# Performance work log

Measured on AMD Instinct MI355X. Metric: run time of the kernel, lower is better.

The kernel has to match this reference:

```python
import jax, jax.numpy as jnp
import numpy as np

B, H, W = 4, 1024, 1024
V, F, T = 98304, 196608, 131072
EPS = 1e-8


def setup_inputs() -> dict:
    key = jax.random.key(0)
    k = jax.random.split(key, 6)
    # screen-space vertices: xy in pixel coords, z (depth) in [0.5, 5.5)
    xy = jax.random.uniform(k[0], (B, V, 2), dtype=jnp.float32) * jnp.array([W, H], jnp.float32)
    z = jax.random.uniform(k[1], (B, V, 1), dtype=jnp.float32) * 5.0 + 0.5
    v2d = jnp.concatenate([xy, z], axis=-1)
    vt = jax.random.uniform(k[2], (T, 2), dtype=jnp.float32)
    vi = jax.random.randint(k[3], (F, 3), 0, V, dtype=jnp.int32)
    vti = jax.random.randint(k[4], (F, 3), 0, T, dtype=jnp.int32)
    # -1 marks background pixels (mask), as in the original renderer
    index_img = jax.random.randint(k[5], (B, H, W), -1, F, dtype=jnp.int32)
    vn = jax.random.normal(jax.random.fold_in(key, 7), (B, V, 3), dtype=jnp.float32)
    return {"v2d": v2d, "vt": vt, "vi": vi, "vti": vti, "index_img": index_img, "vn": vn}


def _epsclamp(x):
    return jnp.where(x < 0, jnp.minimum(x, -EPS), jnp.maximum(x, EPS))


def _gather_b(table, idx):
    # table [B,N,C], idx [B,H,W] -> [B,H,W,C]
    return jax.vmap(lambda t, i: t[i])(table, idx)


def reference(v2d, vt, vi, vti, index_img, vn):
    h, w = index_img.shape[1], index_img.shape[2]
    pcy, pcx = jnp.meshgrid(jnp.arange(h, dtype=v2d.dtype), jnp.arange(w, dtype=v2d.dtype), indexing="ij")
    mask = index_img != -1                       # [B,H,W]
    fm = mask.astype(v2d.dtype)                  # [B,H,W]
    ii = jnp.maximum(index_img, 0)               # [B,H,W]

    vi_img = vi[ii]                              # [B,H,W,3] vertex ids per pixel
    p0 = _gather_b(v2d, vi_img[..., 0])          # [B,H,W,3]
    p1 = _gather_b(v2d, vi_img[..., 1])
    p2 = _gather_b(v2d, vi_img[..., 2])

    vec01 = p1 - p0
    vec02 = p2 - p0
    det = vec01[..., 0] * vec02[..., 1] - vec01[..., 1] * vec02[..., 0]
    denom = _epsclamp(det)
    px = pcx[None] - p0[..., 0]
    py = pcy[None] - p0[..., 1]
    l1 = (px * vec02[..., 1] - py * vec02[..., 0]) / denom
    l2 = (py * vec01[..., 0] - px * vec01[..., 1]) / denom
    l0 = 1.0 - l1 - l2

    w0 = 1.0 / _epsclamp(p0[..., 2])
    w1 = 1.0 / _epsclamp(p1[..., 2])
    w2 = 1.0 / _epsclamp(p2[..., 2])
    zi = 1.0 / _epsclamp(w0 * l0 + w1 * l1 + w2 * l2)
    b0 = w0 * l0 * zi
    b1 = w1 * l1 * zi
    b2 = w2 * l2 * zi
    bary_img = jnp.stack([b0, b1, b2], axis=-1) * fm[..., None]   # [B,H,W,3]

    vti_img = vti[ii]                            # [B,H,W,3]
    t0 = vt[vti_img[..., 0]]                     # [B,H,W,2] (shared uv table)
    t1 = vt[vti_img[..., 1]]
    t2 = vt[vti_img[..., 2]]
    vt_img = t0 * b0[..., None] + t1 * b1[..., None] + t2 * b2[..., None]

    depth_img = zi * fm

    base = jnp.stack([(pcx * 2 + 1) / w, (pcy * 2 + 1) / h], axis=-1) - 1.0  # [H,W,2]
    vt_img = base[None] + fm[..., None] * ((vt_img * 2 - 1) - base[None])    # lerp

    n0 = _gather_b(vn, vi_img[..., 0])
    n1 = _gather_b(vn, vi_img[..., 1])
    n2 = _gather_b(vn, vi_img[..., 2])
    vn_img = (n0 * bary_img[..., 0:1] + n1 * bary_img[..., 1:2] + n2 * bary_img[..., 2:3]) * fm[..., None]

    return depth_img, bary_img, vt_img, vn_img
```

## Files before the change

### kernel.cpp

```cpp
#include <hip/hip_runtime.h>


#define EPSV 1e-8f

__device__ __forceinline__ float epsclamp(float x) {
    return x < 0.0f ? fminf(x, -EPSV) : fmaxf(x, EPSV);
}

constexpr int Wd = 1024, Hd = 1024, Vd = 98304;
constexpr int NPIX = 1 << 22;
constexpr int PPB  = 1 << 20;

struct I3 { int a, b, c; };
struct F3 { float x, y, z; };

__device__ __forceinline__ int base_pixel_swz(int j, int tid) {
    const int xcd = j & 7;
    const int b = xcd >> 1;
    const int sub = ((j >> 3) << 1) + (j & 1);
    return b * PPB + sub * 1024 + tid * 4;
}

__global__ __launch_bounds__(256) void pass1(
    const float* __restrict__ v2d,
    const int*   __restrict__ vi,
    const int*   __restrict__ index_img,
    float* __restrict__ out)
{
#pragma clang fp contract(off)
    const int pb = base_pixel_swz(blockIdx.x, threadIdx.x);
    const int b = pb >> 20;

    const int4 iv = *reinterpret_cast<const int4*>(index_img + pb);
    const int idx[4] = { iv.x, iv.y, iv.z, iv.w };

    I3 ii[4];
#pragma unroll
    for (int k = 0; k < 4; ++k) {
        const int f = idx[k] < 0 ? 0 : idx[k];
        ii[k] = *reinterpret_cast<const I3*>(vi + 3 * (size_t)f);
    }

    const float* __restrict__ vb = v2d + (size_t)b * Vd * 3;
    F3 P0[4], P1[4], P2[4];
#pragma unroll
    for (int k = 0; k < 4; ++k) {
        P0[k] = *reinterpret_cast<const F3*>(vb + 3 * (size_t)ii[k].a);
        P1[k] = *reinterpret_cast<const F3*>(vb + 3 * (size_t)ii[k].b);
        P2[k] = *reinterpret_cast<const F3*>(vb + 3 * (size_t)ii[k].c);
    }

    float dep[4], b0m[4], b1m[4], b2m[4];
#pragma unroll
    for (int k = 0; k < 4; ++k) {
        const int p = pb + k;
        const int x = p & (Wd - 1);
        const int y = (p >> 10) & (Hd - 1);
        const float fm = (idx[k] != -1) ? 1.0f : 0.0f;

        const float v01x = P1[k].x - P0[k].x, v01y = P1[k].y - P0[k].y;
        const float v02x = P2[k].x - P0[k].x, v02y = P2[k].y - P0[k].y;
        const float det = (v01x * v02y) - (v01y * v02x);
        const float denom = epsclamp(det);
        const float pxr = (float)x - P0[k].x;
        const float pyr = (float)y - P0[k].y;
        const float l1 = ((pxr * v02y) - (pyr * v02x)) / denom;
        const float l2 = ((pyr * v01x) - (pxr * v01y)) / denom;
        const float l0 = (1.0f - l1) - l2;

        const float w0 = 1.0f / epsclamp(P0[k].z);
        const float w1 = 1.0f / epsclamp(P1[k].z);
        const float w2 = 1.0f / epsclamp(P2[k].z);
        const float t0w = w0 * l0;
        const float t1w = w1 * l1;
        const float t2w = w2 * l2;
        const float zsum = (t0w + t1w) + t2w;
        const float zi = 1.0f / epsclamp(zsum);

        dep[k] = zi * fm;
        b0m[k] = (t0w * zi) * fm;
        b1m[k] = (t1w * zi) * fm;
        b2m[k] = (t2w * zi) * fm;
    }

    *reinterpret_cast<float4*>(out + pb) = make_float4(dep[0], dep[1], dep[2], dep[3]);
    float* __restrict__ ob = out + (size_t)NPIX + 3 * (size_t)pb;
    reinterpret_cast<float4*>(ob)[0] = make_float4(b0m[0], b1m[0], b2m[0], b0m[1]);
    reinterpret_cast<float4*>(ob)[1] = make_float4(b1m[1], b2m[1], b0m[2], b1m[2]);
    reinterpret_cast<float4*>(ob)[2] = make_float4(b2m[2], b0m[3], b1m[3], b2m[3]);
}

__global__ __launch_bounds__(256) void pass3(
    const float* __restrict__ vn,
    const int*   __restrict__ vi,
    const int*   __restrict__ index_img,
    float* __restrict__ out)
{
#pragma clang fp contract(off)
    const int pb = base_pixel_swz(blockIdx.x, threadIdx.x);
    const int b = pb >> 20;

    const int4 iv = *reinterpret_cast<const int4*>(index_img + pb);
    const int idx[4] = { iv.x, iv.y, iv.z, iv.w };

    I3 ii[4];
#pragma unroll
    for (int k = 0; k < 4; ++k) {
        const int f = idx[k] < 0 ? 0 : idx[k];
        ii[k] = *reinterpret_cast<const I3*>(vi + 3 * (size_t)f);
    }

    const float* __restrict__ nb = vn + (size_t)b * Vd * 3;
    F3 N0[4], N1[4], N2[4];
#pragma unroll
    for (int k = 0; k < 4; ++k) {
        N0[k] = *reinterpret_cast<const F3*>(nb + 3 * (size_t)ii[k].a);
        N1[k] = *reinterpret_cast<const F3*>(nb + 3 * (size_t)ii[k].b);
        N2[k] = *reinterpret_cast<const F3*>(nb + 3 * (size_t)ii[k].c);
    }

    const float* __restrict__ bp = out + (size_t)NPIX + 3 * (size_t)pb;
    const float4 B0 = reinterpret_cast<const float4*>(bp)[0];
    const float4 B1 = reinterpret_cast<const float4*>(bp)[1];
    const float4 B2 = reinterpret_cast<const float4*>(bp)[2];
    const float b0m[4] = { B0.x, B0.w, B1.z, B2.y };
    const float b1m[4] = { B0.y, B1.x, B1.w, B2.z };
    const float b2m[4] = { B0.z, B1.y, B2.x, B2.w };

    float vnx[4], vny[4], vnz[4];
#pragma unroll
    for (int k = 0; k < 4; ++k) {
        const float fm = (idx[k] != -1) ? 1.0f : 0.0f;
        vnx[k] = (((N0[k].x * b0m[k]) + (N1[k].x * b1m[k])) + (N2[k].x * b2m[k])) * fm;
        vny[k] = (((N0[k].y * b0m[k]) + (N1[k].y * b1m[k])) + (N2[k].y * b2m[k])) * fm;
        vnz[k] = (((N0[k].z * b0m[k]) + (N1[k].z * b1m[k])) + (N2[k].z * b2m[k])) * fm;
    }

    float* __restrict__ on = out + (size_t)NPIX * 6 + 3 * (size_t)pb;
    reinterpret_cast<float4*>(on)[0] = make_float4(vnx[0], vny[0], vnz[0], vnx[1]);
    reinterpret_cast<float4*>(on)[1] = make_float4(vny[1], vnz[1], vnx[2], vny[2]);
    reinterpret_cast<float4*>(on)[2] = make_float4(vnz[2], vnx[3], vny[3], vnz[3]);
}

__global__ __launch_bounds__(256) void passB(
    const float* __restrict__ vt,
    const int*   __restrict__ vti,
    const int*   __restrict__ index_img,
    float* __restrict__ out)
{
#pragma clang fp contract(off)
    const int pb = blockIdx.x * 1024 + threadIdx.x * 4;

    const int4 iv = *reinterpret_cast<const int4*>(index_img + pb);
    const int idx[4] = { iv.x, iv.y, iv.z, iv.w };

    I3 tt[4];
#pragma unroll
    for (int k = 0; k < 4; ++k) {
        const int f = idx[k] < 0 ? 0 : idx[k];
        tt[k] = *reinterpret_cast<const I3*>(vti + 3 * (size_t)f);
    }

    const float2* __restrict__ vt2 = reinterpret_cast<const float2*>(vt);
    float2 tA[4], tB[4], tC[4];
#pragma unroll
    for (int k = 0; k < 4; ++k) {
        tA[k] = vt2[tt[k].a];
        tB[k] = vt2[tt[k].b];
        tC[k] = vt2[tt[k].c];
    }

    const float* __restrict__ bp = out + (size_t)NPIX + 3 * (size_t)pb;
    const float4 B0 = reinterpret_cast<const float4*>(bp)[0];
    const float4 B1 = reinterpret_cast<const float4*>(bp)[1];
    const float4 B2 = reinterpret_cast<const float4*>(bp)[2];
    const float b0[4] = { B0.x, B0.w, B1.z, B2.y };
    const float b1[4] = { B0.y, B1.x, B1.w, B2.z };
    const float b2[4] = { B0.z, B1.y, B2.x, B2.w };

    float u[4], v[4];
#pragma unroll
    for (int k = 0; k < 4; ++k) {
        const int p = pb + k;
        const int x = p & (Wd - 1);
        const int y = (p >> 10) & (Hd - 1);
        const float fm = (idx[k] != -1) ? 1.0f : 0.0f;

        float vtx = ((tA[k].x * b0[k]) + (tB[k].x * b1[k])) + (tC[k].x * b2[k]);
        float vty = ((tA[k].y * b0[k]) + (tB[k].y * b1[k])) + (tC[k].y * b2[k]);

        const float bx = (((float)x * 2.0f) + 1.0f) / (float)Wd - 1.0f;
        const float by = (((float)y * 2.0f) + 1.0f) / (float)Hd - 1.0f;
        u[k] = bx + (fm * (((vtx * 2.0f) - 1.0f) - bx));
        v[k] = by + (fm * (((vty * 2.0f) - 1.0f) - by));
    }

    float* __restrict__ ov = out + (size_t)NPIX * 4 + 2 * (size_t)pb;
    reinterpret_cast<float4*>(ov)[0] = make_float4(u[0], v[0], u[1], v[1]);
    reinterpret_cast<float4*>(ov)[1] = make_float4(u[2], v[2], u[3], v[3]);
}

extern "C" void kernel_launch(void* const* d_in, const int* in_sizes, int n_in,
                              void* d_out, int out_size, void* d_ws, size_t ws_size,
                              hipStream_t stream) {
    const float* v2d       = (const float*)d_in[0];
    const float* vt        = (const float*)d_in[1];
    const int*   vi        = (const int*)d_in[2];
    const int*   vti       = (const int*)d_in[3];
    const int*   index_img = (const int*)d_in[4];
    const float* vn        = (const float*)d_in[5];
    float* out = (float*)d_out;

    dim3 grid(NPIX / 1024), block(256);
    pass1<<<grid, block, 0, stream>>>(v2d, vi, index_img, out);
    passB<<<grid, block, 0, stream>>>(vt, vti, index_img, out);
    pass3<<<grid, block, 0, stream>>>(vn, vi, index_img, out);
}
```

Baseline: 249.1 us.

## Repack vertex, face and uv tables to 16-byte aligned records in workspace

```diff
diff --git a/kernel.cpp b/kernel.cpp
--- a/kernel.cpp
+++ b/kernel.cpp
@@ -7,9 +7,21 @@
     return x < 0.0f ? fminf(x, -EPSV) : fmaxf(x, EPSV);
 }
 
-constexpr int Wd = 1024, Hd = 1024, Vd = 98304;
+constexpr int Wd = 1024, Hd = 1024, Vd = 98304, Fd = 196608, Td = 131072, Bd = 4;
 constexpr int NPIX = 1 << 22;
 constexpr int PPB  = 1 << 20;
+
+constexpr size_t OFF_V2DP = 0;
+constexpr size_t SZ_V2DP  = (size_t)Bd * Vd * 16;
+constexpr size_t OFF_VNP  = OFF_V2DP + SZ_V2DP;
+constexpr size_t SZ_VNP   = (size_t)Bd * Vd * 16;
+constexpr size_t OFF_VIP  = OFF_VNP + SZ_VNP;
+constexpr size_t SZ_VIP   = (size_t)Fd * 16;
+constexpr size_t OFF_VTIP = OFF_VIP + SZ_VIP;
+constexpr size_t SZ_VTIP  = (size_t)Fd * 16;
+constexpr size_t OFF_VTP  = OFF_VTIP + SZ_VTIP;
+constexpr size_t SZ_VTP   = (size_t)Td * 16;
+constexpr size_t WS_NEED  = OFF_VTP + SZ_VTP;
 
 struct I3 { int a, b, c; };
 struct F3 { float x, y, z; };
@@ -21,11 +33,34 @@
     return b * PPB + sub * 1024 + tid * 4;
 }
 
-__global__ __launch_bounds__(256) void pass1(
-    const float* __restrict__ v2d,
-    const int*   __restrict__ vi,
-    const int*   __restrict__ index_img,
-    float* __restrict__ out)
+__global__ __launch_bounds__(256) void repack_vert(
+    const float* __restrict__ v2d, const float* __restrict__ vn,
+    float4* __restrict__ v2dp, float4* __restrict__ vnp)
+{
+    const int i = blockIdx.x * 256 + threadIdx.x;
+    v2dp[i] = make_float4(v2d[3 * (size_t)i], v2d[3 * (size_t)i + 1], v2d[3 * (size_t)i + 2], 0.f);
+    vnp[i]  = make_float4(vn[3 * (size_t)i],  vn[3 * (size_t)i + 1],  vn[3 * (size_t)i + 2],  0.f);
+}
+
+__global__ __launch_bounds__(256) void repack_face(
+    const int* __restrict__ vi, const int* __restrict__ vti,
+    int4* __restrict__ vip, int4* __restrict__ vtip)
+{
+    const int f = blockIdx.x * 256 + threadIdx.x;
+    vip[f]  = make_int4(vi[3 * (size_t)f],  vi[3 * (size_t)f + 1],  vi[3 * (size_t)f + 2],  0);
+    vtip[f] = make_int4(vti[3 * (size_t)f], vti[3 * (size_t)f + 1], vti[3 * (size_t)f + 2], 0);
+}
+
+__global__ __launch_bounds__(256) void repack_vt(
+    const float* __restrict__ vt, float4* __restrict__ vtp)
+{
+    const int t = blockIdx.x * 256 + threadIdx.x;
+    vtp[t] = make_float4(vt[2 * (size_t)t], vt[2 * (size_t)t + 1], 0.f, 0.f);
+}
+
+__global__ __launch_bounds__(256) void pass1p(
+    const float4* __restrict__ v2dp, const int4* __restrict__ vip,
+    const int* __restrict__ index_img, float* __restrict__ out)
 {
 #pragma clang fp contract(off)
     const int pb = base_pixel_swz(blockIdx.x, threadIdx.x);
@@ -34,20 +69,20 @@
     const int4 iv = *reinterpret_cast<const int4*>(index_img + pb);
     const int idx[4] = { iv.x, iv.y, iv.z, iv.w };
 
-    I3 ii[4];
-#pragma unroll
-    for (int k = 0; k < 4; ++k) {
-        const int f = idx[k] < 0 ? 0 : idx[k];
-        ii[k] = *reinterpret_cast<const I3*>(vi + 3 * (size_t)f);
-    }
-
-    const float* __restrict__ vb = v2d + (size_t)b * Vd * 3;
-    F3 P0[4], P1[4], P2[4];
-#pragma unroll
-    for (int k = 0; k < 4; ++k) {
-        P0[k] = *reinterpret_cast<const F3*>(vb + 3 * (size_t)ii[k].a);
-        P1[k] = *reinterpret_cast<const F3*>(vb + 3 * (size_t)ii[k].b);
-        P2[k] = *reinterpret_cast<const F3*>(vb + 3 * (size_t)ii[k].c);
+    int4 ii[4];
+#pragma unroll
+    for (int k = 0; k < 4; ++k) {
+        const int f = idx[k] < 0 ? 0 : idx[k];
+        ii[k] = vip[f];
+    }
+
+    const float4* __restrict__ vb = v2dp + (size_t)b * Vd;
+    float4 P0[4], P1[4], P2[4];
+#pragma unroll
+    for (int k = 0; k < 4; ++k) {
+        P0[k] = vb[ii[k].x];
+        P1[k] = vb[ii[k].y];
+        P2[k] = vb[ii[k].z];
     }
 
     float dep[4], b0m[4], b1m[4], b2m[4];
@@ -90,11 +125,9 @@
     reinterpret_cast<float4*>(ob)[2] = make_float4(b2m[2], b0m[3], b1m[3], b2m[3]);
 }
 
-__global__ __launch_bounds__(256) void pass3(
-    const float* __restrict__ vn,
-    const int*   __restrict__ vi,
-    const int*   __restrict__ index_img,
-    float* __restrict__ out)
+__global__ __launch_bounds__(256) void pass3p(
+    const float4* __restrict__ vnp, const int4* __restrict__ vip,
+    const int* __restrict__ index_img, float* __restrict__ out)
 {
 #pragma clang fp contract(off)
     const int pb = base_pixel_swz(blockIdx.x, threadIdx.x);
@@ -103,20 +136,20 @@
     const int4 iv = *reinterpret_cast<const int4*>(index_img + pb);
     const int idx[4] = { iv.x, iv.y, iv.z, iv.w };
 
-    I3 ii[4];
-#pragma unroll
-    for (int k = 0; k < 4; ++k) {
-        const int f = idx[k] < 0 ? 0 : idx[k];
-        ii[k] = *reinterpret_cast<const I3*>(vi + 3 * (size_t)f);
-    }
-
-    const float* __restrict__ nb = vn + (size_t)b * Vd * 3;
-    F3 N0[4], N1[4], N2[4];
-#pragma unroll
-    for (int k = 0; k < 4; ++k) {
-        N0[k] = *reinterpret_cast<const F3*>(nb + 3 * (size_t)ii[k].a);
-        N1[k] = *reinterpret_cast<const F3*>(nb + 3 * (size_t)ii[k].b);
-        N2[k] = *reinterpret_cast<const F3*>(nb + 3 * (size_t)ii[k].c);
+    int4 ii[4];
+#pragma unroll
+    for (int k = 0; k < 4; ++k) {
+        const int f = idx[k] < 0 ? 0 : idx[k];
+        ii[k] = vip[f];
+    }
+
+    const float4* __restrict__ nb = vnp + (size_t)b * Vd;
+    float4 N0[4], N1[4], N2[4];
+#pragma unroll
+    for (int k = 0; k < 4; ++k) {
+        N0[k] = nb[ii[k].x];
+        N1[k] = nb[ii[k].y];
+        N2[k] = nb[ii[k].z];
     }
 
     const float* __restrict__ bp = out + (size_t)NPIX + 3 * (size_t)pb;
@@ -142,11 +175,9 @@
     reinterpret_cast<float4*>(on)[2] = make_float4(vnz[2], vnx[3], vny[3], vnz[3]);
 }
 
-__global__ __launch_bounds__(256) void passB(
-    const float* __restrict__ vt,
-    const int*   __restrict__ vti,
-    const int*   __restrict__ index_img,
-    float* __restrict__ out)
+__global__ __launch_bounds__(256) void passBp(
+    const float4* __restrict__ vtp, const int4* __restrict__ vtip,
+    const int* __restrict__ index_img, float* __restrict__ out)
 {
 #pragma clang fp contract(off)
     const int pb = blockIdx.x * 1024 + threadIdx.x * 4;
@@ -154,20 +185,19 @@
     const int4 iv = *reinterpret_cast<const int4*>(index_img + pb);
     const int idx[4] = { iv.x, iv.y, iv.z, iv.w };
 
-    I3 tt[4];
-#pragma unroll
-    for (int k = 0; k < 4; ++k) {
-        const int f = idx[k] < 0 ? 0 : idx[k];
-        tt[k] = *reinterpret_cast<const I3*>(vti + 3 * (size_t)f);
-    }
-
-    const float2* __restrict__ vt2 = reinterpret_cast<const float2*>(vt);
-    float2 tA[4], tB[4], tC[4];
-#pragma unroll
-    for (int k = 0; k < 4; ++k) {
-        tA[k] = vt2[tt[k].a];
-        tB[k] = vt2[tt[k].b];
-        tC[k] = vt2[tt[k].c];
+    int4 tt[4];
+#pragma unroll
+    for (int k = 0; k < 4; ++k) {
+        const int f = idx[k] < 0 ? 0 : idx[k];
+        tt[k] = vtip[f];
+    }
+
+    float4 tA[4], tB[4], tC[4];
+#pragma unroll
+    for (int k = 0; k < 4; ++k) {
+        tA[k] = vtp[tt[k].x];
+        tB[k] = vtp[tt[k].y];
+        tC[k] = vtp[tt[k].z];
     }
 
     const float* __restrict__ bp = out + (size_t)NPIX + 3 * (size_t)pb;
@@ -195,6 +225,155 @@
         v[k] = by + (fm * (((vty * 2.0f) - 1.0f) - by));
     }
 
+    float* __restrict__ ov = out + (size_t)NPIX * 4 + 2 * (size_t)pb;
+    reinterpret_cast<float4*>(ov)[0] = make_float4(u[0], v[0], u[1], v[1]);
+    reinterpret_cast<float4*>(ov)[1] = make_float4(u[2], v[2], u[3], v[3]);
+}
+
+__global__ __launch_bounds__(256) void pass1f(
+    const float* __restrict__ v2d, const int* __restrict__ vi,
+    const int* __restrict__ index_img, float* __restrict__ out)
+{
+#pragma clang fp contract(off)
+    const int pb = base_pixel_swz(blockIdx.x, threadIdx.x);
+    const int b = pb >> 20;
+    const int4 iv = *reinterpret_cast<const int4*>(index_img + pb);
+    const int idx[4] = { iv.x, iv.y, iv.z, iv.w };
+    I3 ii[4];
+#pragma unroll
+    for (int k = 0; k < 4; ++k) {
+        const int f = idx[k] < 0 ? 0 : idx[k];
+        ii[k] = *reinterpret_cast<const I3*>(vi + 3 * (size_t)f);
+    }
+    const float* __restrict__ vb = v2d + (size_t)b * Vd * 3;
+    F3 P0[4], P1[4], P2[4];
+#pragma unroll
+    for (int k = 0; k < 4; ++k) {
+        P0[k] = *reinterpret_cast<const F3*>(vb + 3 * (size_t)ii[k].a);
+        P1[k] = *reinterpret_cast<const F3*>(vb + 3 * (size_t)ii[k].b);
+        P2[k] = *reinterpret_cast<const F3*>(vb + 3 * (size_t)ii[k].c);
+    }
+    float dep[4], b0m[4], b1m[4], b2m[4];
+#pragma unroll
+    for (int k = 0; k < 4; ++k) {
+        const int p = pb + k;
+        const int x = p & (Wd - 1);
+        const int y = (p >> 10) & (Hd - 1);
+        const float fm = (idx[k] != -1) ? 1.0f : 0.0f;
+        const float v01x = P1[k].x - P0[k].x, v01y = P1[k].y - P0[k].y;
+        const float v02x = P2[k].x - P0[k].x, v02y = P2[k].y - P0[k].y;
+        const float det = (v01x * v02y) - (v01y * v02x);
+        const float denom = epsclamp(det);
+        const float pxr = (float)x - P0[k].x;
+        const float pyr = (float)y - P0[k].y;
+        const float l1 = ((pxr * v02y) - (pyr * v02x)) / denom;
+        const float l2 = ((pyr * v01x) - (pxr * v01y)) / denom;
+        const float l0 = (1.0f - l1) - l2;
+        const float w0 = 1.0f / epsclamp(P0[k].z);
+        const float w1 = 1.0f / epsclamp(P1[k].z);
+        const float w2 = 1.0f / epsclamp(P2[k].z);
+        const float t0w = w0 * l0, t1w = w1 * l1, t2w = w2 * l2;
+        const float zsum = (t0w + t1w) + t2w;
+        const float zi = 1.0f / epsclamp(zsum);
+        dep[k] = zi * fm;
+        b0m[k] = (t0w * zi) * fm;
+        b1m[k] = (t1w * zi) * fm;
+        b2m[k] = (t2w * zi) * fm;
+    }
+    *reinterpret_cast<float4*>(out + pb) = make_float4(dep[0], dep[1], dep[2], dep[3]);
+    float* __restrict__ ob = out + (size_t)NPIX + 3 * (size_t)pb;
+    reinterpret_cast<float4*>(ob)[0] = make_float4(b0m[0], b1m[0], b2m[0], b0m[1]);
+    reinterpret_cast<float4*>(ob)[1] = make_float4(b1m[1], b2m[1], b0m[2], b1m[2]);
+    reinterpret_cast<float4*>(ob)[2] = make_float4(b2m[2], b0m[3], b1m[3], b2m[3]);
+}
+
+__global__ __launch_bounds__(256) void pass3f(
+    const float* __restrict__ vn, const int* __restrict__ vi,
+    const int* __restrict__ index_img, float* __restrict__ out)
+{
+#pragma clang fp contract(off)
+    const int pb = base_pixel_swz(blockIdx.x, threadIdx.x);
+    const int b = pb >> 20;
+    const int4 iv = *reinterpret_cast<const int4*>(index_img + pb);
+    const int idx[4] = { iv.x, iv.y, iv.z, iv.w };
+    I3 ii[4];
+#pragma unroll
+    for (int k = 0; k < 4; ++k) {
+        const int f = idx[k] < 0 ? 0 : idx[k];
+        ii[k] = *reinterpret_cast<const I3*>(vi + 3 * (size_t)f);
+    }
+    const float* __restrict__ nb = vn + (size_t)b * Vd * 3;
+    F3 N0[4], N1[4], N2[4];
+#pragma unroll
+    for (int k = 0; k < 4; ++k) {
+        N0[k] = *reinterpret_cast<const F3*>(nb + 3 * (size_t)ii[k].a);
+        N1[k] = *reinterpret_cast<const F3*>(nb + 3 * (size_t)ii[k].b);
+        N2[k] = *reinterpret_cast<const F3*>(nb + 3 * (size_t)ii[k].c);
+    }
+    const float* __restrict__ bp = out + (size_t)NPIX + 3 * (size_t)pb;
+    const float4 B0 = reinterpret_cast<const float4*>(bp)[0];
+    const float4 B1 = reinterpret_cast<const float4*>(bp)[1];
+    const float4 B2 = reinterpret_cast<const float4*>(bp)[2];
+    const float b0m[4] = { B0.x, B0.w, B1.z, B2.y };
+    const float b1m[4] = { B0.y, B1.x, B1.w, B2.z };
+    const float b2m[4] = { B0.z, B1.y, B2.x, B2.w };
+    float vnx[4], vny[4], vnz[4];
+#pragma unroll
+    for (int k = 0; k < 4; ++k) {
+        const float fm = (idx[k] != -1) ? 1.0f : 0.0f;
+        vnx[k] = (((N0[k].x * b0m[k]) + (N1[k].x * b1m[k])) + (N2[k].x * b2m[k])) * fm;
+        vny[k] = (((N0[k].y * b0m[k]) + (N1[k].y * b1m[k])) + (N2[k].y * b2m[k])) * fm;
+        vnz[k] = (((N0[k].z * b0m[k]) + (N1[k].z * b1m[k])) + (N2[k].z * b2m[k])) * fm;
+    }
+    float* __restrict__ on = out + (size_t)NPIX * 6 + 3 * (size_t)pb;
+    reinterpret_cast<float4*>(on)[0] = make_float4(vnx[0], vny[0], vnz[0], vnx[1]);
+    reinterpret_cast<float4*>(on)[1] = make_float4(vny[1], vnz[1], vnx[2], vny[2]);
+    reinterpret_cast<float4*>(on)[2] = make_float4(vnz[2], vnx[3], vny[3], vnz[3]);
+}
+
+__global__ __launch_bounds__(256) void passBf(
+    const float* __restrict__ vt, const int* __restrict__ vti,
+    const int* __restrict__ index_img, float* __restrict__ out)
+{
+#pragma clang fp contract(off)
+    const int pb = blockIdx.x * 1024 + threadIdx.x * 4;
+    const int4 iv = *reinterpret_cast<const int4*>(index_img + pb);
+    const int idx[4] = { iv.x, iv.y, iv.z, iv.w };
+    I3 tt[4];
+#pragma unroll
+    for (int k = 0; k < 4; ++k) {
+        const int f = idx[k] < 0 ? 0 : idx[k];
+        tt[k] = *reinterpret_cast<const I3*>(vti + 3 * (size_t)f);
+    }
+    const float2* __restrict__ vt2 = reinterpret_cast<const float2*>(vt);
+    float2 tA[4], tB[4], tC[4];
+#pragma unroll
+    for (int k = 0; k < 4; ++k) {
+        tA[k] = vt2[tt[k].a];
+        tB[k] = vt2[tt[k].b];
+        tC[k] = vt2[tt[k].c];
+    }
+    const float* __restrict__ bp = out + (size_t)NPIX + 3 * (size_t)pb;
+    const float4 B0 = reinterpret_cast<const float4*>(bp)[0];
+    const float4 B1 = reinterpret_cast<const float4*>(bp)[1];
+    const float4 B2 = reinterpret_cast<const float4*>(bp)[2];
+    const float b0[4] = { B0.x, B0.w, B1.z, B2.y };
+    const float b1[4] = { B0.y, B1.x, B1.w, B2.z };
+    const float b2[4] = { B0.z, B1.y, B2.x, B2.w };
+    float u[4], v[4];
+#pragma unroll
+    for (int k = 0; k < 4; ++k) {
+        const int p = pb + k;
+        const int x = p & (Wd - 1);
+        const int y = (p >> 10) & (Hd - 1);
+        const float fm = (idx[k] != -1) ? 1.0f : 0.0f;
+        float vtx = ((tA[k].x * b0[k]) + (tB[k].x * b1[k])) + (tC[k].x * b2[k]);
+        float vty = ((tA[k].y * b0[k]) + (tB[k].y * b1[k])) + (tC[k].y * b2[k]);
+        const float bx = (((float)x * 2.0f) + 1.0f) / (float)Wd - 1.0f;
+        const float by = (((float)y * 2.0f) + 1.0f) / (float)Hd - 1.0f;
+        u[k] = bx + (fm * (((vtx * 2.0f) - 1.0f) - bx));
+        v[k] = by + (fm * (((vty * 2.0f) - 1.0f) - by));
+    }
     float* __restrict__ ov = out + (size_t)NPIX * 4 + 2 * (size_t)pb;
     reinterpret_cast<float4*>(ov)[0] = make_float4(u[0], v[0], u[1], v[1]);
     reinterpret_cast<float4*>(ov)[1] = make_float4(u[2], v[2], u[3], v[3]);
@@ -211,8 +390,27 @@
     const float* vn        = (const float*)d_in[5];
     float* out = (float*)d_out;
 
-    dim3 grid(NPIX / 1024), block(256);
-    pass1<<<grid, block, 0, stream>>>(v2d, vi, index_img, out);
-    passB<<<grid, block, 0, stream>>>(vt, vti, index_img, out);
-    pass3<<<grid, block, 0, stream>>>(vn, vi, index_img, out);
-}
+    dim3 block(256);
+    dim3 gridPx(NPIX / 1024);
+
+    if (ws_size >= WS_NEED) {
+        char* ws = (char*)d_ws;
+        float4* v2dp = (float4*)(ws + OFF_V2DP);
+        float4* vnp  = (float4*)(ws + OFF_VNP);
+        int4*   vip  = (int4*)(ws + OFF_VIP);
+        int4*   vtip = (int4*)(ws + OFF_VTIP);
+        float4* vtp  = (float4*)(ws + OFF_VTP);
+
+        repack_vert<<<dim3(Bd * Vd / 256), block, 0, stream>>>(v2d, vn, v2dp, vnp);
+        repack_face<<<dim3(Fd / 256), block, 0, stream>>>(vi, vti, vip, vtip);
+        repack_vt  <<<dim3(Td / 256), block, 0, stream>>>(vt, vtp);
+
+        pass1p<<<gridPx, block, 0, stream>>>(v2dp, vip, index_img, out);
+        passBp<<<gridPx, block, 0, stream>>>(vtp, vtip, index_img, out);
+        pass3p<<<gridPx, block, 0, stream>>>(vnp, vip, index_img, out);
+    } else {
+        pass1f<<<gridPx, block, 0, stream>>>(v2d, vi, index_img, out);
+        passBf<<<gridPx, block, 0, stream>>>(vt, vti, index_img, out);
+        pass3f<<<gridPx, block, 0, stream>>>(vn, vi, index_img, out);
+    }
+}
```

Measured after the change: 280.7 us. +12.7%, slower.
